# Kernel tuning notes

Measured on AMD Instinct MI355X. Metric: run time of the kernel, lower is better.

## Reference

```python
import jax, jax.numpy as jnp
import numpy as np

D_MODEL = 1024
NUM_HEADS = 16
D_K = D_MODEL // NUM_HEADS


def setup_inputs() -> dict:
    key = jax.random.key(0)
    ks = jax.random.split(key, 11)
    B, S = 2, 2048
    scale = 1.0 / np.sqrt(D_MODEL)
    inp = {
        "Q": jax.random.normal(ks[0], (B, S, D_MODEL), jnp.float32),
        "K": jax.random.normal(ks[1], (B, S, D_MODEL), jnp.float32),
        "V": jax.random.normal(ks[2], (B, S, D_MODEL), jnp.float32),
        # per-head projection weights stacked on head axis: [H, d_model, d_k]
        "Wq": jax.random.uniform(ks[3], (NUM_HEADS, D_MODEL, D_K), jnp.float32, -scale, scale),
        "bq": jax.random.uniform(ks[4], (NUM_HEADS, D_K), jnp.float32, -scale, scale),
        "Wk": jax.random.uniform(ks[5], (NUM_HEADS, D_MODEL, D_K), jnp.float32, -scale, scale),
        "bk": jax.random.uniform(ks[6], (NUM_HEADS, D_K), jnp.float32, -scale, scale),
        "Wv": jax.random.uniform(ks[7], (NUM_HEADS, D_MODEL, D_K), jnp.float32, -scale, scale),
        "bv": jax.random.uniform(ks[8], (NUM_HEADS, D_K), jnp.float32, -scale, scale),
        "Wo": jax.random.uniform(ks[9], (D_MODEL, D_MODEL), jnp.float32, -scale, scale),
        "bo": jax.random.uniform(ks[10], (D_MODEL,), jnp.float32, -scale, scale),
    }
    return inp


def reference(Q, K, V, Wq, bq, Wk, bk, Wv, bv, Wo, bo):
    # Batched equivalent of the per-head loop: project all heads at once.
    q = jnp.einsum("bsd,hdk->bhsk", Q, Wq) + bq[None, :, None, :]
    k = jnp.einsum("bsd,hdk->bhsk", K, Wk) + bk[None, :, None, :]
    v = jnp.einsum("bsd,hdk->bhsk", V, Wv) + bv[None, :, None, :]
    scores = jnp.einsum("bhqk,bhmk->bhqm", q, k) / jnp.sqrt(jnp.float32(D_K))
    weights = jax.nn.softmax(scores, axis=-1)
    attn = jnp.einsum("bhqm,bhmk->bhqk", weights, v)  # [B,H,S,d_k]
    B, H, S, Dk = attn.shape
    concat = attn.transpose(0, 2, 1, 3).reshape(B, S, H * Dk)  # head-order concat
    return concat @ Wo.T + bo
```

## Files before the change

### kernel.cpp

```cpp
#include <hip/hip_runtime.h>
#include <math.h>

#define BATCH 2
#define SLEN 2048
#define DM 1024
#define NH 16
#define DK 64
#define STILES (SLEN / 64)

typedef __attribute__((ext_vector_type(8))) __bf16 bf16x8;
typedef __attribute__((ext_vector_type(4))) float f32x4;

__device__ __forceinline__ unsigned short f2bf(float x) {
  unsigned u = __builtin_bit_cast(unsigned, x);
  unsigned r = (u + 0x7fffu + ((u >> 16) & 1u)) >> 16;
  return (unsigned short)r;
}
__device__ __forceinline__ void splitbf(float x, unsigned short& h,
                                        unsigned short& l) {
  unsigned u = __builtin_bit_cast(unsigned, x);
  h = (unsigned short)(u >> 16);
  float hf = __builtin_bit_cast(float, u & 0xffff0000u);
  l = (unsigned short)(__builtin_bit_cast(unsigned, x - hf) >> 16);
}

__device__ __forceinline__ void gld16(const unsigned short* g,
                                      unsigned short* l) {
  __builtin_amdgcn_global_load_lds(
      (const __attribute__((address_space(1))) void*)g,
      (__attribute__((address_space(3))) void*)l, 16, 0, 0);
}

__global__ __launch_bounds__(256)
void convert_w(const float* __restrict__ Wq, const float* __restrict__ Wk,
               const float* __restrict__ Wv, unsigned short* __restrict__ Wqt,
               unsigned short* __restrict__ Wkt,
               unsigned short* __restrict__ Wvt) {
  const int kb = blockIdx.x, h = blockIdx.y, z = blockIdx.z;
  const float* W = (z == 0 ? Wq : z == 1 ? Wk : Wv) +
                   ((size_t)h * DM + kb * 64) * DK;
  unsigned short* D = (z == 0 ? Wqt : z == 1 ? Wkt : Wvt);

  __shared__ float T[64][65];
  const int tid = threadIdx.x;
  {
    int r = tid >> 2, c0 = (tid & 3) * 16;
#pragma unroll
    for (int i = 0; i < 4; ++i) {
      float4 f = *(const float4*)(W + (size_t)r * DK + c0 + i * 4);
      T[r][c0 + i * 4 + 0] = f.x;
      T[r][c0 + i * 4 + 1] = f.y;
      T[r][c0 + i * 4 + 2] = f.z;
      T[r][c0 + i * 4 + 3] = f.w;
    }
  }
  __syncthreads();
  int j = tid >> 2, p = tid & 3;
  int n = h * 64 + j;
  int kloc = p * 16;
  unsigned short hi[16], lo[16];
#pragma unroll
  for (int i = 0; i < 16; ++i) splitbf(T[kloc + i][j], hi[i], lo[i]);
  int kglob = kb * 64 + kloc;
  int blk = kglob >> 5;
  int c0 = (kglob & 31) >> 3;
  int key = n & 7;
  unsigned short* rowp = D + (size_t)n * 2048 + blk * 64;
  uint4 u0, u1;
  u0.x = (unsigned)hi[0] | ((unsigned)hi[1] << 16);
  u0.y = (unsigned)hi[2] | ((unsigned)hi[3] << 16);
  u0.z = (unsigned)hi[4] | ((unsigned)hi[5] << 16);
  u0.w = (unsigned)hi[6] | ((unsigned)hi[7] << 16);
  u1.x = (unsigned)hi[8] | ((unsigned)hi[9] << 16);
  u1.y = (unsigned)hi[10] | ((unsigned)hi[11] << 16);
  u1.z = (unsigned)hi[12] | ((unsigned)hi[13] << 16);
  u1.w = (unsigned)hi[14] | ((unsigned)hi[15] << 16);
  *(uint4*)(rowp + ((c0 ^ key)) * 8) = u0;
  *(uint4*)(rowp + (((c0 + 1) ^ key)) * 8) = u1;
  u0.x = (unsigned)lo[0] | ((unsigned)lo[1] << 16);
  u0.y = (unsigned)lo[2] | ((unsigned)lo[3] << 16);
  u0.z = (unsigned)lo[4] | ((unsigned)lo[5] << 16);
  u0.w = (unsigned)lo[6] | ((unsigned)lo[7] << 16);
  u1.x = (unsigned)lo[8] | ((unsigned)lo[9] << 16);
  u1.y = (unsigned)lo[10] | ((unsigned)lo[11] << 16);
  u1.z = (unsigned)lo[12] | ((unsigned)lo[13] << 16);
  u1.w = (unsigned)lo[14] | ((unsigned)lo[15] << 16);
  *(uint4*)(rowp + (((c0 + 4) ^ key)) * 8) = u0;
  *(uint4*)(rowp + (((c0 + 5) ^ key)) * 8) = u1;
}

__global__ __launch_bounds__(256)
void convert_x(const float* __restrict__ Q, const float* __restrict__ K,
               const float* __restrict__ V, unsigned short* __restrict__ Xp) {
  const int m = blockIdx.x, z = blockIdx.y;
  const float* src = (z == 0 ? Q : z == 1 ? K : V) + (size_t)m * DM;
  unsigned short* dst =
      Xp + (size_t)z * (8u * 1024 * 1024) + (size_t)m * 2048;
  const int k0 = threadIdx.x * 4;
  float4 f = *(const float4*)(src + k0);
  ushort4 h4, l4;
  splitbf(f.x, h4.x, l4.x);
  splitbf(f.y, h4.y, l4.y);
  splitbf(f.z, h4.z, l4.z);
  splitbf(f.w, h4.w, l4.w);
  int blk = k0 >> 5, ch = (k0 & 31) >> 3, off = k0 & 7, key = m & 7;
  unsigned short* rowp = dst + blk * 64;
  *(ushort4*)(rowp + ((ch ^ key)) * 8 + off) = h4;
  *(ushort4*)(rowp + (((ch + 4) ^ key)) * 8 + off) = l4;
}

__global__ __launch_bounds__(256)
void convert_wo(const float* __restrict__ Wo, unsigned short* __restrict__ Wot) {
  const int n = blockIdx.x;
  const int t = threadIdx.x;
  const int k0 = t * 4;
  float4 f = *(const float4*)(Wo + (size_t)n * DM + k0);
  ushort4 h4, l4;
  splitbf(f.x, h4.x, l4.x);
  splitbf(f.y, h4.y, l4.y);
  splitbf(f.z, h4.z, l4.z);
  splitbf(f.w, h4.w, l4.w);
  int blk = k0 >> 5, ch = (k0 & 31) >> 3, off = k0 & 7, key = n & 7;
  unsigned short* rowp = Wot + (size_t)n * 2048 + blk * 64;
  *(ushort4*)(rowp + ((ch ^ key)) * 8 + off) = h4;
  *(ushort4*)(rowp + (((ch + 4) ^ key)) * 8 + off) = l4;
}

__global__ __launch_bounds__(512, 2)
void proj_gemm(const unsigned short* __restrict__ Xp,
               const unsigned short* __restrict__ Wqt,
               const unsigned short* __restrict__ Wkt,
               const unsigned short* __restrict__ Wvt,
               const float* __restrict__ bq, const float* __restrict__ bk,
               const float* __restrict__ bv, unsigned short* __restrict__ q_all,
               unsigned short* __restrict__ k_all,
               unsigned short* __restrict__ vt) {
  const int ntile = blockIdx.x, mt = blockIdx.y, z = blockIdx.z;
  const unsigned short* Bw = (z == 0 ? Wqt : z == 1 ? Wkt : Wvt);
  const float* bias = (z == 0 ? bq : z == 1 ? bk : bv);

  __shared__ alignas(16) unsigned short As[2][256 * 64];
  __shared__ alignas(16) unsigned short Bs[2][256 * 64];

  const int tid = threadIdx.x;
  const int lane = tid & 63, w = tid >> 6;
  const int l15 = lane & 15, quad = lane >> 4;
  const int wm = (w >> 2) * 128, wn = (w & 3) * 64;
  const int kx = l15 & 7;
  const int r0 = tid >> 3, seg = tid & 7;

  const unsigned short* Ap =
      Xp + (size_t)z * (8u * 1024 * 1024) + (size_t)(mt * 256) * 2048;
  const unsigned short* Bp = Bw + (size_t)(ntile * 256) * 2048;

#define STAGE_A(bf, hh, t)                                                    \
  do {                                                                        \
    const unsigned short* _s =                                                \
        Ap + (size_t)((hh)*64 + r0) * 2048 + (t)*64 + seg * 8;                \
    unsigned short* _d = &As[bf][((hh)*64 + r0) * 64 + seg * 8];              \
    gld16(_s, _d);                                                            \
    gld16(_s + (size_t)128 * 2048, _d + 128 * 64);                            \
  } while (0)
#define STAGE_B(bf, hh, t)                                                    \
  do {                                                                        \
    int _rb = ((r0 >> 5) << 6) + (hh)*32 + (r0 & 31);                         \
    const unsigned short* _s = Bp + (size_t)_rb * 2048 + (t)*64 + seg * 8;    \
    unsigned short* _d = &Bs[bf][_rb * 64 + seg * 8];                         \
    gld16(_s, _d);                                                            \
    gld16(_s + (size_t)128 * 2048, _d + 128 * 64);                            \
  } while (0)
#define VMW(n) asm volatile("s_waitcnt vmcnt(" #n ")" ::: "memory")

#define PHASE(BUF, QM, QN, STG, VMS)                                          \
  do {                                                                        \
    bf16x8 ah_[4], al_[4], bh_[2], bl_[2];                                    \
    _Pragma("unroll") for (int i_ = 0; i_ < 4; ++i_) {                        \
      const unsigned short* p_ =                                              \
          &As[BUF][(wm + (QM)*64 + i_ * 16 + l15) * 64];                      \
      ah_[i_] = *(const bf16x8*)(p_ + ((quad ^ kx)) * 8);                     \
      al_[i_] = *(const bf16x8*)(p_ + (((quad + 4) ^ kx)) * 8);               \
    }                                                                         \
    _Pragma("unroll") for (int j_ = 0; j_ < 2; ++j_) {                        \
      const unsigned short* p_ =                                              \
          &Bs[BUF][(wn + (QN)*32 + j_ * 16 + l15) * 64];                      \
      bh_[j_] = *(const bf16x8*)(p_ + ((quad ^ kx)) * 8);                     \
      bl_[j_] = *(const bf16x8*)(p_ + (((quad + 4) ^ kx)) * 8);               \
    }                                                                         \
    STG;                                                                      \
    VMS;                                                                      \
    asm volatile("s_waitcnt lgkmcnt(8)" ::: "memory");                        \
    __builtin_amdgcn_s_barrier();                                             \
    asm volatile("s_waitcnt lgkmcnt(0)" ::: "memory");                        \
    __builtin_amdgcn_sched_barrier(0);                                        \
    __builtin_amdgcn_s_setprio(1);                                            \
    _Pragma("unroll") for (int j_ = 0; j_ < 2; ++j_)                          \
        _Pragma("unroll") for (int i_ = 0; i_ < 4; ++i_) {                    \
      acc[QM][QN][i_][j_] = __builtin_amdgcn_mfma_f32_16x16x32_bf16(          \
          ah_[i_], bh_[j_], acc[QM][QN][i_][j_], 0, 0, 0);                    \
      acc[QM][QN][i_][j_] = __builtin_amdgcn_mfma_f32_16x16x32_bf16(          \
          al_[i_], bh_[j_], acc[QM][QN][i_][j_], 0, 0, 0);                    \
      acc[QM][QN][i_][j_] = __builtin_amdgcn_mfma_f32_16x16x32_bf16(          \
          ah_[i_], bl_[j_], acc[QM][QN][i_][j_], 0, 0, 0);                    \
    }                                                                         \
    __builtin_amdgcn_s_setprio(0);                                            \
    __builtin_amdgcn_sched_barrier(0);                                        \
    __builtin_amdgcn_s_barrier();                                             \
  } while (0)

  f32x4 acc[2][2][4][2];
#pragma unroll
  for (int a0 = 0; a0 < 2; ++a0)
#pragma unroll
    for (int a1 = 0; a1 < 2; ++a1)
#pragma unroll
      for (int a2 = 0; a2 < 4; ++a2)
#pragma unroll
        for (int a3 = 0; a3 < 2; ++a3)
          acc[a0][a1][a2][a3] = (f32x4){0.f, 0.f, 0.f, 0.f};

  STAGE_B(0, 0, 0);
  STAGE_A(0, 0, 0);
  STAGE_A(0, 1, 0);
  STAGE_B(0, 1, 0);
  STAGE_B(1, 0, 1);
  STAGE_A(1, 0, 1);
  VMW(4);
  __builtin_amdgcn_s_barrier();

#pragma unroll 1
  for (int it2 = 0; it2 < 16; ++it2) {
    const int O = 2 * it2 + 1;
    const int En = 2 * it2 + 2;
    const int On = 2 * it2 + 3;
    const bool sE = (it2 < 15);
    PHASE(0, 0, 0, STAGE_A(1, 1, O), (void)0);
    PHASE(0, 1, 0, STAGE_B(1, 1, O), (void)0);
    PHASE(0, 0, 1, if (sE) STAGE_B(0, 0, En), (void)0);
    PHASE(0, 1, 1, if (sE) STAGE_A(0, 0, En),
          if (sE) { VMW(4); } else { VMW(0); });
    PHASE(1, 0, 0, if (sE) STAGE_A(0, 1, En), (void)0);
    PHASE(1, 1, 0, if (sE) STAGE_B(0, 1, En), (void)0);
    PHASE(1, 0, 1, if (sE) STAGE_B(1, 0, On), (void)0);
    PHASE(1, 1, 1, if (sE) STAGE_A(1, 0, On), if (sE) VMW(4));
  }
#undef PHASE
#undef VMW
#undef STAGE_A
#undef STAGE_B

  if (z <= 1) {
    unsigned short* dst = (z == 0 ? q_all : k_all);
#pragma unroll
    for (int qm = 0; qm < 2; ++qm)
#pragma unroll
      for (int qn = 0; qn < 2; ++qn)
#pragma unroll
        for (int i = 0; i < 4; ++i)
#pragma unroll
          for (int j = 0; j < 2; ++j) {
            int n = ntile * 256 + wn + qn * 32 + j * 16 + l15;
            int hh_ = n >> 6, d = n & 63;
            int chi = (d >> 5) * 8 + ((d & 31) >> 3);
            float bn = bias[n];
#pragma unroll
            for (int r = 0; r < 4; ++r) {
              int m = mt * 256 + wm + qm * 64 + i * 16 + quad * 4 + r;
              int key = m & 15;
              size_t rb = (size_t)m * 2048 + hh_ * 128;
              unsigned short hv, lv;
              splitbf(acc[qm][qn][i][j][r] + bn, hv, lv);
              dst[rb + ((chi ^ key)) * 8 + (d & 7)] = hv;
              dst[rb + (((chi + 4) ^ key)) * 8 + (d & 7)] = lv;
            }
          }
  } else {
#pragma unroll
    for (int qm = 0; qm < 2; ++qm)
#pragma unroll
      for (int qn = 0; qn < 2; ++qn)
#pragma unroll
        for (int i = 0; i < 4; ++i)
#pragma unroll
          for (int j = 0; j < 2; ++j) {
            int n = ntile * 256 + wn + qn * 32 + j * 16 + l15;
            int h = n >> 6, d = n & 63;
            float bn = bias[n];
            int m0 = mt * 256 + wm + qm * 64 + i * 16 + quad * 4;
            int b = m0 >> 11, s0_ = m0 & 2047;
            int kt = s0_ >> 6, sl = s0_ & 63;
            int ch = sl >> 3, off = sl & 7, key = d & 15;
            ushort4 h4, l4;
            splitbf(acc[qm][qn][i][j][0] + bn, h4.x, l4.x);
            splitbf(acc[qm][qn][i][j][1] + bn, h4.y, l4.y);
            splitbf(acc[qm][qn][i][j][2] + bn, h4.z, l4.z);
            splitbf(acc[qm][qn][i][j][3] + bn, h4.w, l4.w);
            size_t base =
                (size_t)(b * NH + h) * 262144 + (size_t)d * 4096 + kt * 128;
            *(ushort4*)(vt + base + ((ch ^ key)) * 8 + off) = h4;
            *(ushort4*)(vt + base + (((ch + 8) ^ key)) * 8 + off) = l4;
          }
  }
}

__global__ __launch_bounds__(256)
void out_gemm(const unsigned short* __restrict__ a_all,
              const unsigned short* __restrict__ Wot,
              const float* __restrict__ bo, float* __restrict__ out) {
  const int ntile = blockIdx.x, mt = blockIdx.y;

  __shared__ alignas(16) unsigned short As[2][64 * 64];
  __shared__ alignas(16) unsigned short Bs[2][128 * 64];

  const int tid = threadIdx.x;
  const int lane = tid & 63, w = tid >> 6;
  const int l15 = lane & 15, quad = lane >> 4;
  const int wn = w * 32;
  const int kx = l15 & 7;

  const unsigned short* Ap = a_all + (size_t)(mt * 64) * 2048;
  const unsigned short* Bp = Wot + (size_t)(ntile * 128) * 2048;

#pragma unroll
  for (int it = 0; it < 2; ++it) {
    int s = tid + it * 256;
    int r = s >> 3, seg = s & 7;
    gld16(Ap + (size_t)r * 2048 + seg * 8, &As[0][s * 8]);
  }
#pragma unroll
  for (int it = 0; it < 4; ++it) {
    int s = tid + it * 256;
    int r = s >> 3, seg = s & 7;
    gld16(Bp + (size_t)r * 2048 + seg * 8, &Bs[0][s * 8]);
  }

  f32x4 acc[4][2];
#pragma unroll
  for (int i = 0; i < 4; ++i)
#pragma unroll
    for (int j = 0; j < 2; ++j) acc[i][j] = (f32x4){0.f, 0.f, 0.f, 0.f};

  int cur = 0;
  for (int kk = 0; kk < 32; ++kk) {
    __syncthreads();

    if (kk + 1 < 32) {
      int blk = (kk + 1) * 64;
#pragma unroll
      for (int it = 0; it < 2; ++it) {
        int s = tid + it * 256;
        int r = s >> 3, seg = s & 7;
        gld16(Ap + (size_t)r * 2048 + blk + seg * 8, &As[cur ^ 1][s * 8]);
      }
#pragma unroll
      for (int it = 0; it < 4; ++it) {
        int s = tid + it * 256;
        int r = s >> 3, seg = s & 7;
        gld16(Bp + (size_t)r * 2048 + blk + seg * 8, &Bs[cur ^ 1][s * 8]);
      }
    }

    bf16x8 ah[4], al[4];
#pragma unroll
    for (int i = 0; i < 4; ++i) {
      const unsigned short* p = &As[cur][(i * 16 + l15) * 64];
      ah[i] = *(const bf16x8*)(p + ((quad ^ kx)) * 8);
      al[i] = *(const bf16x8*)(p + (((quad + 4) ^ kx)) * 8);
    }
#pragma unroll
    for (int j = 0; j < 2; ++j) {
      const unsigned short* p = &Bs[cur][(wn + j * 16 + l15) * 64];
      bf16x8 bh = *(const bf16x8*)(p + ((quad ^ kx)) * 8);
      bf16x8 bl = *(const bf16x8*)(p + (((quad + 4) ^ kx)) * 8);
#pragma unroll
      for (int i = 0; i < 4; ++i) {
        acc[i][j] = __builtin_amdgcn_mfma_f32_16x16x32_bf16(ah[i], bh, acc[i][j], 0, 0, 0);
        acc[i][j] = __builtin_amdgcn_mfma_f32_16x16x32_bf16(al[i], bh, acc[i][j], 0, 0, 0);
        acc[i][j] = __builtin_amdgcn_mfma_f32_16x16x32_bf16(ah[i], bl, acc[i][j], 0, 0, 0);
      }
    }
    cur ^= 1;
  }

#pragma unroll
  for (int i = 0; i < 4; ++i)
#pragma unroll
    for (int j = 0; j < 2; ++j) {
      int n = ntile * 128 + wn + j * 16 + l15;
      float bn = bo[n];
#pragma unroll
      for (int r = 0; r < 4; ++r) {
        int m = mt * 64 + i * 16 + quad * 4 + r;
        out[(size_t)m * DM + n] = acc[i][j][r] + bn;
      }
    }
}

__global__ __launch_bounds__(256)
void attn_kernel(const unsigned short* __restrict__ q_all,
                 const unsigned short* __restrict__ k_all,
                 const unsigned short* __restrict__ vt,
                 unsigned short* __restrict__ a_all) {
  const int qt = blockIdx.x, h = blockIdx.y, b = blockIdx.z;
  const unsigned short* vp = vt + (size_t)(b * NH + h) * 262144;

  __shared__ alignas(16) unsigned short Ks[2][64 * 128];
  __shared__ alignas(16) unsigned short Vs[2][64 * 128];
  __shared__ alignas(16) unsigned short Ps[128 * 64];

  const int tid = threadIdx.x;
  const int lane = tid & 63;
  const int w = tid >> 6;
  const int l15 = lane & 15;
  const int quad = lane >> 4;

  bf16x8 qf[2][2][2];
#pragma unroll
  for (int rt = 0; rt < 2; ++rt) {
    const unsigned short* qrow =
        q_all + (size_t)(b * SLEN + qt * 128 + w * 32 + rt * 16 + l15) * 2048 +
        h * 128;
#pragma unroll
    for (int kb = 0; kb < 2; ++kb) {
      qf[rt][kb][0] = *(const bf16x8*)(qrow + ((kb * 8 + quad) ^ l15) * 8);
      qf[rt][kb][1] = *(const bf16x8*)(qrow + ((kb * 8 + quad + 4) ^ l15) * 8);
    }
  }

  {
    const unsigned short* ksrc = k_all + (size_t)(b * SLEN) * 2048 + h * 128;
#pragma unroll
    for (int it = 0; it < 4; ++it) {
      int ss = it * 256 + tid;
      int r = ss >> 4, p = ss & 15;
      gld16(ksrc + (size_t)r * 2048 + p * 8, &Ks[0][ss * 8]);
    }
#pragma unroll
    for (int it = 0; it < 4; ++it) {
      int ss = it * 256 + tid;
      int d = ss >> 4, p = ss & 15;
      gld16(vp + (size_t)d * 4096 + p * 8, &Vs[0][ss * 8]);
    }
  }

  f32x4 o[2][4];
  float lpart[2][4];
#pragma unroll
  for (int rt = 0; rt < 2; ++rt)
#pragma unroll
    for (int nt = 0; nt < 4; ++nt) {
      o[rt][nt] = (f32x4){0.f, 0.f, 0.f, 0.f};
      lpart[rt][nt] = 0.f;
    }

  int cur = 0;
  for (int kt = 0; kt < STILES; ++kt) {
    __syncthreads();

    if (kt + 1 < STILES) {
      const unsigned short* ksrc =
          k_all + (size_t)(b * SLEN + (kt + 1) * 64) * 2048 + h * 128;
#pragma unroll
      for (int it = 0; it < 4; ++it) {
        int ss = it * 256 + tid;
        int r = ss >> 4, p = ss & 15;
        gld16(ksrc + (size_t)r * 2048 + p * 8, &Ks[cur ^ 1][ss * 8]);
      }
#pragma unroll
      for (int it = 0; it < 4; ++it) {
        int ss = it * 256 + tid;
        int d = ss >> 4, p = ss & 15;
        gld16(vp + (size_t)d * 4096 + (kt + 1) * 128 + p * 8,
              &Vs[cur ^ 1][ss * 8]);
      }
    }

    f32x4 sc[2][4];
#pragma unroll
    for (int rt = 0; rt < 2; ++rt)
#pragma unroll
      for (int ct = 0; ct < 4; ++ct) sc[rt][ct] = (f32x4){0.f, 0.f, 0.f, 0.f};
    __builtin_amdgcn_s_setprio(1);
#pragma unroll
    for (int ct = 0; ct < 4; ++ct) {
      const unsigned short* kbase = &Ks[cur][(ct * 16 + l15) * 128];
#pragma unroll
      for (int kb = 0; kb < 2; ++kb) {
        bf16x8 kh = *(const bf16x8*)(kbase + ((kb * 8 + quad) ^ l15) * 8);
        bf16x8 kl = *(const bf16x8*)(kbase + ((kb * 8 + quad + 4) ^ l15) * 8);
#pragma unroll
        for (int rt = 0; rt < 2; ++rt) {
          sc[rt][ct] = __builtin_amdgcn_mfma_f32_16x16x32_bf16(qf[rt][kb][0], kh, sc[rt][ct], 0, 0, 0);
          sc[rt][ct] = __builtin_amdgcn_mfma_f32_16x16x32_bf16(qf[rt][kb][0], kl, sc[rt][ct], 0, 0, 0);
          sc[rt][ct] = __builtin_amdgcn_mfma_f32_16x16x32_bf16(qf[rt][kb][1], kh, sc[rt][ct], 0, 0, 0);
        }
      }
    }
    __builtin_amdgcn_s_setprio(0);

#pragma unroll
    for (int rt = 0; rt < 2; ++rt)
#pragma unroll
      for (int ct = 0; ct < 4; ++ct)
#pragma unroll
        for (int r = 0; r < 4; ++r) {
          float e = __expf(sc[rt][ct][r] * 0.125f);
          lpart[rt][r] += e;
          int prow = w * 32 + rt * 16 + quad * 4 + r;
          int pkey = (prow >> 1) & 7;
          Ps[prow * 64 + (((ct * 2 + (l15 >> 3)) ^ pkey)) * 8 + (l15 & 7)] =
              f2bf(e);
        }
    asm volatile("s_waitcnt lgkmcnt(0)" ::: "memory");
    __builtin_amdgcn_sched_barrier(0);

    int rk = (l15 >> 1) & 7;
#pragma unroll
    for (int kb = 0; kb < 2; ++kb) {
      bf16x8 pf[2];
#pragma unroll
      for (int rt = 0; rt < 2; ++rt)
        pf[rt] = *(const bf16x8*)(&Ps[(w * 32 + rt * 16 + l15) * 64 +
                                      (((kb * 4 + quad) ^ rk)) * 8]);
      __builtin_amdgcn_s_setprio(1);
#pragma unroll
      for (int nt = 0; nt < 4; ++nt) {
        const unsigned short* vb = &Vs[cur][(nt * 16 + l15) * 128];
        bf16x8 vh = *(const bf16x8*)(vb + (((kb * 4 + quad) ^ l15)) * 8);
        bf16x8 vl = *(const bf16x8*)(vb + (((kb * 4 + quad + 8) ^ l15)) * 8);
#pragma unroll
        for (int rt = 0; rt < 2; ++rt) {
          o[rt][nt] = __builtin_amdgcn_mfma_f32_16x16x32_bf16(pf[rt], vh, o[rt][nt], 0, 0, 0);
          o[rt][nt] = __builtin_amdgcn_mfma_f32_16x16x32_bf16(pf[rt], vl, o[rt][nt], 0, 0, 0);
        }
      }
      __builtin_amdgcn_s_setprio(0);
    }
    cur ^= 1;
  }

#pragma unroll
  for (int rt = 0; rt < 2; ++rt) {
    float inv[4];
#pragma unroll
    for (int r = 0; r < 4; ++r) {
      float lv = lpart[rt][r];
#pragma unroll
      for (int m = 1; m < 16; m <<= 1) lv += __shfl_xor(lv, m, 64);
      inv[r] = 1.f / lv;
    }
#pragma unroll
    for (int nt = 0; nt < 4; ++nt) {
      int c = h * 64 + nt * 16 + l15;
      int Bb = c >> 5;
      int d32 = c & 31;
      int ch = d32 >> 3, off = d32 & 7;
#pragma unroll
      for (int r = 0; r < 4; ++r) {
        float val = o[rt][nt][r] * inv[r];
        int srow = qt * 128 + w * 32 + rt * 16 + quad * 4 + r;
        int key = srow & 7;
        size_t g = (size_t)(b * SLEN + srow) * 2048 + Bb * 64;
        unsigned short hv, lv2;
        splitbf(val, hv, lv2);
        a_all[g + ((ch ^ key)) * 8 + off] = hv;
        a_all[g + (((ch + 4) ^ key)) * 8 + off] = lv2;
      }
    }
  }
}

extern "C" void kernel_launch(void* const* d_in, const int* in_sizes, int n_in,
                              void* d_out, int out_size, void* d_ws,
                              size_t ws_size, hipStream_t stream) {
  (void)in_sizes; (void)n_in; (void)out_size; (void)ws_size;
  const float* Q = (const float*)d_in[0];
  const float* K = (const float*)d_in[1];
  const float* V = (const float*)d_in[2];
  const float* Wq = (const float*)d_in[3];
  const float* bq = (const float*)d_in[4];
  const float* Wk = (const float*)d_in[5];
  const float* bk = (const float*)d_in[6];
  const float* Wv = (const float*)d_in[7];
  const float* bv = (const float*)d_in[8];
  const float* Wo = (const float*)d_in[9];
  const float* bo = (const float*)d_in[10];
  float* out = (float*)d_out;

  unsigned short* us = (unsigned short*)d_ws;
  const size_t M8 = 8u * 1024 * 1024;
  unsigned short* q_all = us;
  unsigned short* k_all = us + M8;
  unsigned short* vt = us + 2 * M8;
  unsigned short* a_all = us + 3 * M8;
  unsigned short* Wqt = a_all;
  unsigned short* Wkt = a_all + 2 * 1024 * 1024;
  unsigned short* Wvt = a_all + 4 * 1024 * 1024;
  unsigned short* Xp = us + 4 * M8;
  unsigned short* Wot = q_all;

  convert_w<<<dim3(16, 16, 3), 256, 0, stream>>>(Wq, Wk, Wv, Wqt, Wkt, Wvt);
  convert_x<<<dim3(4096, 3), 256, 0, stream>>>(Q, K, V, Xp);
  proj_gemm<<<dim3(4, 16, 3), 512, 0, stream>>>(Xp, Wqt, Wkt, Wvt, bq, bk, bv,
                                                q_all, k_all, vt);
  attn_kernel<<<dim3(SLEN / 128, NH, BATCH), 256, 0, stream>>>(q_all, k_all,
                                                               vt, a_all);
  convert_wo<<<dim3(1024), 256, 0, stream>>>(Wo, Wot);
  out_gemm<<<dim3(8, 64), 256, 0, stream>>>(a_all, Wot, bo, out);
}
```

Measured before the change: 347.5 us.

## Shrink attention tiles to 64 queries and 32 keys for higher occupancy

The attention kernel now handles 64 query rows per block (16 per wave) and steps over 32-key tiles, so the grid doubles to 1024 blocks. Shared memory and register use per block drop, and launch bounds request 4 blocks per CU. The V staging uses a new swizzle to take 32-key halves out of the 64-wide transposed layout. The cost is twice the K/V global traffic per query row and twice as many loop iterations and barriers.

```diff
diff --git a/kernel.cpp b/kernel.cpp
--- a/kernel.cpp
+++ b/kernel.cpp
@@ -6,7 +6,6 @@
 #define DM 1024
 #define NH 16
 #define DK 64
-#define STILES (SLEN / 64)
 
 typedef __attribute__((ext_vector_type(8))) __bf16 bf16x8;
 typedef __attribute__((ext_vector_type(4))) float f32x4;
@@ -395,7 +394,7 @@
     }
 }
 
-__global__ __launch_bounds__(256)
+__global__ __launch_bounds__(256, 4)
 void attn_kernel(const unsigned short* __restrict__ q_all,
                  const unsigned short* __restrict__ k_all,
                  const unsigned short* __restrict__ vt,
@@ -403,9 +402,9 @@
   const int qt = blockIdx.x, h = blockIdx.y, b = blockIdx.z;
   const unsigned short* vp = vt + (size_t)(b * NH + h) * 262144;
 
-  __shared__ alignas(16) unsigned short Ks[2][64 * 128];
-  __shared__ alignas(16) unsigned short Vs[2][64 * 128];
-  __shared__ alignas(16) unsigned short Ps[128 * 64];
+  __shared__ alignas(16) unsigned short Ks[2][32 * 128];
+  __shared__ alignas(16) unsigned short Vs[2][64 * 64];
+  __shared__ alignas(16) unsigned short Ps[64 * 32];
 
   const int tid = threadIdx.x;
   const int lane = tid & 63;
@@ -413,158 +412,128 @@
   const int l15 = lane & 15;
   const int quad = lane >> 4;
 
-  bf16x8 qf[2][2][2];
-#pragma unroll
-  for (int rt = 0; rt < 2; ++rt) {
+  bf16x8 qf[2][2];
+  {
     const unsigned short* qrow =
-        q_all + (size_t)(b * SLEN + qt * 128 + w * 32 + rt * 16 + l15) * 2048 +
-        h * 128;
+        q_all + (size_t)(b * SLEN + qt * 64 + w * 16 + l15) * 2048 + h * 128;
 #pragma unroll
     for (int kb = 0; kb < 2; ++kb) {
-      qf[rt][kb][0] = *(const bf16x8*)(qrow + ((kb * 8 + quad) ^ l15) * 8);
-      qf[rt][kb][1] = *(const bf16x8*)(qrow + ((kb * 8 + quad + 4) ^ l15) * 8);
-    }
-  }
-
-  {
-    const unsigned short* ksrc = k_all + (size_t)(b * SLEN) * 2048 + h * 128;
-#pragma unroll
-    for (int it = 0; it < 4; ++it) {
-      int ss = it * 256 + tid;
-      int r = ss >> 4, p = ss & 15;
-      gld16(ksrc + (size_t)r * 2048 + p * 8, &Ks[0][ss * 8]);
-    }
-#pragma unroll
-    for (int it = 0; it < 4; ++it) {
-      int ss = it * 256 + tid;
-      int d = ss >> 4, p = ss & 15;
-      gld16(vp + (size_t)d * 4096 + p * 8, &Vs[0][ss * 8]);
-    }
-  }
-
-  f32x4 o[2][4];
-  float lpart[2][4];
-#pragma unroll
-  for (int rt = 0; rt < 2; ++rt)
-#pragma unroll
-    for (int nt = 0; nt < 4; ++nt) {
-      o[rt][nt] = (f32x4){0.f, 0.f, 0.f, 0.f};
-      lpart[rt][nt] = 0.f;
-    }
+      qf[kb][0] = *(const bf16x8*)(qrow + ((kb * 8 + quad) ^ l15) * 8);
+      qf[kb][1] = *(const bf16x8*)(qrow + ((kb * 8 + quad + 4) ^ l15) * 8);
+    }
+  }
+
+#define STAGE_KV(kt_, buf_)                                                   \
+  do {                                                                        \
+    const unsigned short* ksrc =                                              \
+        k_all + (size_t)(b * SLEN + (kt_)*32) * 2048 + h * 128;               \
+    _Pragma("unroll") for (int it = 0; it < 2; ++it) {                        \
+      int ss = it * 256 + tid;                                                \
+      int r = ss >> 4, p = ss & 15;                                           \
+      gld16(ksrc + (size_t)r * 2048 + p * 8, &Ks[buf_][ss * 8]);              \
+    }                                                                         \
+    int t64 = (kt_) >> 1, h32 = (kt_)&1;                                      \
+    _Pragma("unroll") for (int it = 0; it < 2; ++it) {                        \
+      int ss = it * 256 + tid;                                                \
+      int d = ss >> 3, p = ss & 7;                                            \
+      int l = p ^ (d & 7);                                                    \
+      int c = (l < 4 ? h32 * 4 + l : 4 + h32 * 4 + l);                        \
+      gld16(vp + (size_t)d * 4096 + t64 * 128 + ((c ^ (d & 15))) * 8,         \
+            &Vs[buf_][ss * 8]);                                               \
+    }                                                                         \
+  } while (0)
+
+  STAGE_KV(0, 0);
+
+  f32x4 o[4];
+  float lpart[4];
+#pragma unroll
+  for (int nt = 0; nt < 4; ++nt) o[nt] = (f32x4){0.f, 0.f, 0.f, 0.f};
+#pragma unroll
+  for (int r = 0; r < 4; ++r) lpart[r] = 0.f;
 
   int cur = 0;
-  for (int kt = 0; kt < STILES; ++kt) {
+#pragma unroll 1
+  for (int kt = 0; kt < 64; ++kt) {
     __syncthreads();
 
-    if (kt + 1 < STILES) {
-      const unsigned short* ksrc =
-          k_all + (size_t)(b * SLEN + (kt + 1) * 64) * 2048 + h * 128;
-#pragma unroll
-      for (int it = 0; it < 4; ++it) {
-        int ss = it * 256 + tid;
-        int r = ss >> 4, p = ss & 15;
-        gld16(ksrc + (size_t)r * 2048 + p * 8, &Ks[cur ^ 1][ss * 8]);
-      }
-#pragma unroll
-      for (int it = 0; it < 4; ++it) {
-        int ss = it * 256 + tid;
-        int d = ss >> 4, p = ss & 15;
-        gld16(vp + (size_t)d * 4096 + (kt + 1) * 128 + p * 8,
-              &Vs[cur ^ 1][ss * 8]);
-      }
-    }
-
-    f32x4 sc[2][4];
-#pragma unroll
-    for (int rt = 0; rt < 2; ++rt)
-#pragma unroll
-      for (int ct = 0; ct < 4; ++ct) sc[rt][ct] = (f32x4){0.f, 0.f, 0.f, 0.f};
+    if (kt + 1 < 64) STAGE_KV(kt + 1, cur ^ 1);
+
+    f32x4 sc[2];
+#pragma unroll
+    for (int ct = 0; ct < 2; ++ct) sc[ct] = (f32x4){0.f, 0.f, 0.f, 0.f};
     __builtin_amdgcn_s_setprio(1);
 #pragma unroll
-    for (int ct = 0; ct < 4; ++ct) {
+    for (int ct = 0; ct < 2; ++ct) {
       const unsigned short* kbase = &Ks[cur][(ct * 16 + l15) * 128];
 #pragma unroll
       for (int kb = 0; kb < 2; ++kb) {
         bf16x8 kh = *(const bf16x8*)(kbase + ((kb * 8 + quad) ^ l15) * 8);
         bf16x8 kl = *(const bf16x8*)(kbase + ((kb * 8 + quad + 4) ^ l15) * 8);
-#pragma unroll
-        for (int rt = 0; rt < 2; ++rt) {
-          sc[rt][ct] = __builtin_amdgcn_mfma_f32_16x16x32_bf16(qf[rt][kb][0], kh, sc[rt][ct], 0, 0, 0);
-          sc[rt][ct] = __builtin_amdgcn_mfma_f32_16x16x32_bf16(qf[rt][kb][0], kl, sc[rt][ct], 0, 0, 0);
-          sc[rt][ct] = __builtin_amdgcn_mfma_f32_16x16x32_bf16(qf[rt][kb][1], kh, sc[rt][ct], 0, 0, 0);
-        }
+        sc[ct] = __builtin_amdgcn_mfma_f32_16x16x32_bf16(qf[kb][0], kh, sc[ct], 0, 0, 0);
+        sc[ct] = __builtin_amdgcn_mfma_f32_16x16x32_bf16(qf[kb][0], kl, sc[ct], 0, 0, 0);
+        sc[ct] = __builtin_amdgcn_mfma_f32_16x16x32_bf16(qf[kb][1], kh, sc[ct], 0, 0, 0);
       }
     }
     __builtin_amdgcn_s_setprio(0);
 
 #pragma unroll
-    for (int rt = 0; rt < 2; ++rt)
-#pragma unroll
-      for (int ct = 0; ct < 4; ++ct)
-#pragma unroll
-        for (int r = 0; r < 4; ++r) {
-          float e = __expf(sc[rt][ct][r] * 0.125f);
-          lpart[rt][r] += e;
-          int prow = w * 32 + rt * 16 + quad * 4 + r;
-          int pkey = (prow >> 1) & 7;
-          Ps[prow * 64 + (((ct * 2 + (l15 >> 3)) ^ pkey)) * 8 + (l15 & 7)] =
-              f2bf(e);
-        }
+    for (int ct = 0; ct < 2; ++ct)
+#pragma unroll
+      for (int r = 0; r < 4; ++r) {
+        float e = __expf(sc[ct][r] * 0.125f);
+        lpart[r] += e;
+        int prow = w * 16 + quad * 4 + r;
+        int pk = (prow >> 1) & 3;
+        Ps[prow * 32 + (((ct * 2 + (l15 >> 3)) ^ pk)) * 8 + (l15 & 7)] =
+            f2bf(e);
+      }
     asm volatile("s_waitcnt lgkmcnt(0)" ::: "memory");
     __builtin_amdgcn_sched_barrier(0);
 
-    int rk = (l15 >> 1) & 7;
-#pragma unroll
-    for (int kb = 0; kb < 2; ++kb) {
-      bf16x8 pf[2];
-#pragma unroll
-      for (int rt = 0; rt < 2; ++rt)
-        pf[rt] = *(const bf16x8*)(&Ps[(w * 32 + rt * 16 + l15) * 64 +
-                                      (((kb * 4 + quad) ^ rk)) * 8]);
+    {
+      int rk = (l15 >> 1) & 3;
+      bf16x8 pf =
+          *(const bf16x8*)(&Ps[(w * 16 + l15) * 32 + ((quad ^ rk)) * 8]);
       __builtin_amdgcn_s_setprio(1);
 #pragma unroll
       for (int nt = 0; nt < 4; ++nt) {
-        const unsigned short* vb = &Vs[cur][(nt * 16 + l15) * 128];
-        bf16x8 vh = *(const bf16x8*)(vb + (((kb * 4 + quad) ^ l15)) * 8);
-        bf16x8 vl = *(const bf16x8*)(vb + (((kb * 4 + quad + 8) ^ l15)) * 8);
-#pragma unroll
-        for (int rt = 0; rt < 2; ++rt) {
-          o[rt][nt] = __builtin_amdgcn_mfma_f32_16x16x32_bf16(pf[rt], vh, o[rt][nt], 0, 0, 0);
-          o[rt][nt] = __builtin_amdgcn_mfma_f32_16x16x32_bf16(pf[rt], vl, o[rt][nt], 0, 0, 0);
-        }
+        const unsigned short* vb = &Vs[cur][(nt * 16 + l15) * 64];
+        bf16x8 vh = *(const bf16x8*)(vb + ((quad ^ (l15 & 7))) * 8);
+        bf16x8 vl = *(const bf16x8*)(vb + (((quad + 4) ^ (l15 & 7))) * 8);
+        o[nt] = __builtin_amdgcn_mfma_f32_16x16x32_bf16(pf, vh, o[nt], 0, 0, 0);
+        o[nt] = __builtin_amdgcn_mfma_f32_16x16x32_bf16(pf, vl, o[nt], 0, 0, 0);
       }
       __builtin_amdgcn_s_setprio(0);
     }
     cur ^= 1;
   }
-
-#pragma unroll
-  for (int rt = 0; rt < 2; ++rt) {
-    float inv[4];
+#undef STAGE_KV
+
+  float inv[4];
+#pragma unroll
+  for (int r = 0; r < 4; ++r) {
+    float lv = lpart[r];
+#pragma unroll
+    for (int m = 1; m < 16; m <<= 1) lv += __shfl_xor(lv, m, 64);
+    inv[r] = 1.f / lv;
+  }
+#pragma unroll
+  for (int nt = 0; nt < 4; ++nt) {
+    int c = h * 64 + nt * 16 + l15;
+    int Bb = c >> 5;
+    int d32 = c & 31;
+    int ch = d32 >> 3, off = d32 & 7;
 #pragma unroll
     for (int r = 0; r < 4; ++r) {
-      float lv = lpart[rt][r];
-#pragma unroll
-      for (int m = 1; m < 16; m <<= 1) lv += __shfl_xor(lv, m, 64);
-      inv[r] = 1.f / lv;
-    }
-#pragma unroll
-    for (int nt = 0; nt < 4; ++nt) {
-      int c = h * 64 + nt * 16 + l15;
-      int Bb = c >> 5;
-      int d32 = c & 31;
-      int ch = d32 >> 3, off = d32 & 7;
-#pragma unroll
-      for (int r = 0; r < 4; ++r) {
-        float val = o[rt][nt][r] * inv[r];
-        int srow = qt * 128 + w * 32 + rt * 16 + quad * 4 + r;
-        int key = srow & 7;
-        size_t g = (size_t)(b * SLEN + srow) * 2048 + Bb * 64;
-        unsigned short hv, lv2;
-        splitbf(val, hv, lv2);
-        a_all[g + ((ch ^ key)) * 8 + off] = hv;
-        a_all[g + (((ch + 4) ^ key)) * 8 + off] = lv2;
-      }
+      float val = o[nt][r] * inv[r];
+      int srow = qt * 64 + w * 16 + quad * 4 + r;
+      int key = srow & 7;
+      size_t g = (size_t)(b * SLEN + srow) * 2048 + Bb * 64;
+      unsigned short hv, lv2;
+      splitbf(val, hv, lv2);
+      a_all[g + ((ch ^ key)) * 8 + off] = hv;
+      a_all[g + (((ch + 4) ^ key)) * 8 + off] = lv2;
     }
   }
 }
@@ -602,8 +571,8 @@
   convert_x<<<dim3(4096, 3), 256, 0, stream>>>(Q, K, V, Xp);
   proj_gemm<<<dim3(4, 16, 3), 512, 0, stream>>>(Xp, Wqt, Wkt, Wvt, bq, bk, bv,
                                                 q_all, k_all, vt);
-  attn_kernel<<<dim3(SLEN / 128, NH, BATCH), 256, 0, stream>>>(q_all, k_all,
-                                                               vt, a_all);
+  attn_kernel<<<dim3(SLEN / 64, NH, BATCH), 256, 0, stream>>>(q_all, k_all,
+                                                              vt, a_all);
   convert_wo<<<dim3(1024), 256, 0, stream>>>(Wo, Wot);
   out_gemm<<<dim3(8, 64), 256, 0, stream>>>(a_all, Wot, bo, out);
 }
```

Measured after the change: 367.3 us. 5.7% more time.
